# Kernel tuning notes

Hardware: AMD Instinct MI355X
Metric: run time of the kernel (lower is better)

## Reference

```python
import jax, jax.numpy as jnp
import numpy as np

SPATIAL_SCALE = 0.125  # stride-8 FPN level
POINTS = 5


def _sample_points(bb):
    # bb: [N,H,W,5] = (cx, cy, w, h, theta) in image coords
    cx, cy, w, h, t = [bb[..., i] for i in range(5)]
    if POINTS == 1:
        px = cx[..., None]
        py = cy[..., None]
    else:
        vx = w * jnp.cos(t) * 0.5
        vy = w * jnp.sin(t) * 0.5
        wx = -h * jnp.sin(t) * 0.5
        wy = h * jnp.cos(t) * 0.5
        px = jnp.stack([cx, cx + vx + wx, cx - vx + wx, cx - vx - wx, cx + vx - wx], axis=-1)
        py = jnp.stack([cy, cy + vy + wy, cy - vy + wy, cy - vy - wy, cy + vy - wy], axis=-1)
    return px * SPATIAL_SCALE, py * SPATIAL_SCALE  # [N,H,W,P] feature-map coords


def _bilinear_gather(feat, y, x):
    # feat: [N,C,H,W]; y,x: [N,H,W,P] -> [N,H,W,P,C], mmcv-style bilinear w/ border rules
    N, C, H, W = feat.shape
    valid = (y >= -1.0) & (y <= H) & (x >= -1.0) & (x <= W)
    y = jnp.maximum(y, 0.0)
    x = jnp.maximum(x, 0.0)
    y_low = jnp.minimum(jnp.floor(y).astype(jnp.int32), H - 1)
    x_low = jnp.minimum(jnp.floor(x).astype(jnp.int32), W - 1)
    # if low index hits last row/col, snap coordinate onto it (ly/lx = 0)
    y = jnp.where(y_low >= H - 1, y_low.astype(feat.dtype), y)
    x = jnp.where(x_low >= W - 1, x_low.astype(feat.dtype), x)
    y_high = jnp.minimum(y_low + 1, H - 1)
    x_high = jnp.minimum(x_low + 1, W - 1)
    ly = y - y_low.astype(feat.dtype)
    lx = x - x_low.astype(feat.dtype)
    hy = 1.0 - ly
    hx = 1.0 - lx
    nn = jnp.arange(N)[:, None, None, None]  # broadcasts against [N,H,W,P]

    def g(yy, xx):
        return feat[nn, :, yy, xx]  # [N,H,W,P,C]

    val = ((hy * hx)[..., None] * g(y_low, x_low)
           + (hy * lx)[..., None] * g(y_low, x_high)
           + (ly * hx)[..., None] * g(y_high, x_low)
           + (ly * lx)[..., None] * g(y_high, x_high))
    return jnp.where(valid[..., None], val, 0.0)


def feature_refine(features, best_rbboxes):
    px, py = _sample_points(best_rbboxes)
    sampled = _bilinear_gather(features, py, px)       # [N,H,W,P,C]
    acc = sampled.sum(axis=3)                           # [N,H,W,C]
    return features + jnp.transpose(acc, (0, 3, 1, 2))  # [N,C,H,W]


def setup_inputs() -> dict:
    key = jax.random.key(0)
    k1, k2, k3, k4, k5, k6 = jax.random.split(key, 6)
    N, C, H, W = 4, 256, 128, 128
    IMG = 1024.0
    features = jax.random.normal(k1, (N, C, H, W), dtype=jnp.float32)
    cx = jax.random.uniform(k2, (N, H, W), minval=0.0, maxval=IMG)
    cy = jax.random.uniform(k3, (N, H, W), minval=0.0, maxval=IMG)
    bw = jax.random.uniform(k4, (N, H, W), minval=8.0, maxval=128.0)
    bh = jax.random.uniform(k5, (N, H, W), minval=8.0, maxval=128.0)
    th = jax.random.uniform(k6, (N, H, W), minval=-np.pi / 2, maxval=np.pi / 2)
    best_rbboxes = jnp.stack([cx, cy, bw, bh, th], axis=-1)  # [N,H,W,5]
    return {"features": features, "best_rbboxes": best_rbboxes}


def reference(features, best_rbboxes):
    return feature_refine(features, best_rbboxes)
```

## Files before the change

### kernel.cpp

```cpp
#include <hip/hip_runtime.h>


#define N_ 4
#define C_ 256
#define H_ 128
#define W_ 128
#define HW_ (H_ * W_)
#define SCALE 0.125f

typedef unsigned int uint32;

__device__ __forceinline__ uint32 f2bf(float f) {
    uint32 u = __float_as_uint(f);
    u = (u + 0x7FFF + ((u >> 16) & 1)) >> 16;
    return u;
}
__device__ __forceinline__ float blo(uint32 u) { return __uint_as_float(u << 16); }
__device__ __forceinline__ float bhi(uint32 u) { return __uint_as_float(u & 0xFFFF0000u); }

__global__ __launch_bounds__(1024, 8) void nchw2nhwc_geo(const float* __restrict__ in,
                                                         const float* __restrict__ bb,
                                                         uint32* __restrict__ outU,
                                                         uint32* __restrict__ geoG)
{
    __shared__ uint32 tile[64 * 260];
    const int t   = threadIdx.x;
    const int l   = t & 63;
    const int g   = t >> 6;
    const int hw0 = blockIdx.x * 256;
    const int ch  = blockIdx.y;
    const int n   = blockIdx.z;

    if (ch == 0 && t < 256) {
        const int px = n * HW_ + hw0 + t;
        const float* b = bb + (size_t)px * 5;
        const float cx = b[0], cy = b[1], bw = b[2], bh = b[3], th = b[4];
        const float st = sinf(th), ct = cosf(th);
        const float vx = bw * ct * 0.5f, vy = bw * st * 0.5f;
        const float wx = -bh * st * 0.5f, wy = bh * ct * 0.5f;
        const float pxs[5] = {cx, cx + vx + wx, cx - vx + wx, cx - vx - wx, cx + vx - wx};
        const float pys[5] = {cy, cy + vy + wy, cy - vy + wy, cy - vy - wy, cy + vy - wy};
        uint32* gw = geoG + (size_t)px * 32;
#pragma unroll
        for (int p = 0; p < 5; ++p) {
            float x = pxs[p] * SCALE;
            float y = pys[p] * SCALE;
            const bool valid = (y >= -1.0f) && (y <= (float)H_) &&
                               (x >= -1.0f) && (x <= (float)W_);
            y = fmaxf(y, 0.0f);
            x = fmaxf(x, 0.0f);
            int yl = min((int)y, H_ - 1);
            int xl = min((int)x, W_ - 1);
            if (yl >= H_ - 1) y = (float)yl;
            if (xl >= W_ - 1) x = (float)xl;
            const int yh = min(yl + 1, H_ - 1);
            const float ly = y - (float)yl, lx = x - (float)xl;
            const float hy = 1.0f - ly,     hx = 1.0f - lx;
            const int xa = min(xl, W_ - 2);
            float wA, wB;
            if (xl < W_ - 1) { wA = hx; wB = lx; }
            else             { wA = 0.0f; wB = 1.0f; }
            const float v = valid ? 1.0f : 0.0f;
            gw[p]      = (uint32)(yl * W_ + xa);
            gw[5 + p]  = (uint32)(yh * W_ + xa);
            gw[10 + p] = __float_as_uint(v * hy * wA);
            gw[15 + p] = __float_as_uint(v * hy * wB);
            gw[20 + p] = __float_as_uint(v * ly * wA);
            gw[25 + p] = __float_as_uint(v * ly * wB);
        }
        gw[30] = 0u; gw[31] = 0u;
    }

    const float* base = in + (size_t)n * C_ * HW_ + (size_t)(ch * 128) * HW_ + hw0 + 4 * l;
    float4 v0[4], v1[4];
#pragma unroll
    for (int r = 0; r < 4; ++r) {
        const int cp = g * 4 + r;
        v0[r] = *(const float4*)(base + (size_t)(2 * cp) * HW_);
        v1[r] = *(const float4*)(base + (size_t)(2 * cp + 1) * HW_);
    }
#pragma unroll
    for (int r = 0; r < 4; ++r) {
        const int cp = g * 4 + r;
        uint4 u;
        u.x = f2bf(v0[r].x) | (f2bf(v1[r].x) << 16);
        u.y = f2bf(v0[r].y) | (f2bf(v1[r].y) << 16);
        u.z = f2bf(v0[r].z) | (f2bf(v1[r].z) << 16);
        u.w = f2bf(v0[r].w) | (f2bf(v1[r].w) << 16);
        *(uint4*)&tile[cp * 260 + 4 * l] = u;
    }
    __syncthreads();
    uint32* dst = outU + ((size_t)n * HW_ + hw0) * 128 + ch * 64;
#pragma unroll
    for (int it = 0; it < 16; ++it) {
        const int f   = it * 1024 + t;
        const int row = f >> 6;
        const int q   = f & 63;
        dst[(size_t)row * 128 + q] = tile[q * 260 + row];
    }
}

__global__ __launch_bounds__(256, 8) void fr_refine(const uint32* __restrict__ nhwcU,
                                                    const uint32* __restrict__ geoG,
                                                    float* __restrict__ out)
{
    __shared__ float tile[32 * 128];
    const int t  = threadIdx.x;
    const int l  = t & 63;
    const int wv = __builtin_amdgcn_readfirstlane(t >> 6);
    const int bx = blockIdx.x;
    const int xcd = bx & 7;
    const int n   = xcd >> 1;
    const int ch  = xcd & 1;
    const int s   = bx >> 3;
    const int h   = s >> 2;
    const int w0  = (s & 3) * 32;

    const int chB = ch << 8;
    const int laneb = ((l & 15) << 4) + (((l >> 4) & 1) << 9);
    const bool hi = (l >= 32);
    const bool b4 = ((l >> 4) & 1) != 0;
    const int hwb = h * W_ + w0 + wv * 8;
    const uint32* gb = geoG + ((size_t)n * HW_ + hwb) * 32;
    const char* plane = (const char*)(nhwcU + (size_t)n * HW_ * 128);

#pragma unroll 1
    for (int p = 0; p < 8; ++p) {
        const uint32* g = gb + p * 32;

        int o0b[5], o1b[5];
        float w00[5], w01[5], w10[5], w11[5];
#pragma unroll
        for (int q = 0; q < 5; ++q) {
            o0b[q] = (int)__builtin_amdgcn_readfirstlane(g[q])     * 512 + chB;
            o1b[q] = (int)__builtin_amdgcn_readfirstlane(g[5 + q]) * 512 + chB;
            w00[q] = __uint_as_float(__builtin_amdgcn_readfirstlane(g[10 + q]));
            w01[q] = __uint_as_float(__builtin_amdgcn_readfirstlane(g[15 + q]));
            w10[q] = __uint_as_float(__builtin_amdgcn_readfirstlane(g[20 + q]));
            w11[q] = __uint_as_float(__builtin_amdgcn_readfirstlane(g[25 + q]));
        }

        uint4 rid = make_uint4(0u, 0u, 0u, 0u);
        if (l < 16)
            rid = *(const uint4*)(plane + (size_t)(hwb + p) * 512 + chB + ((l & 15) << 4));
        uint4 r[5];
#pragma unroll
        for (int q = 0; q < 5; ++q) {
            const int vof = (hi ? o1b[q] : o0b[q]) + laneb;
            r[q] = *(const uint4*)(plane + vof);
        }
        __builtin_amdgcn_sched_barrier(0);

        float a[8];
        a[0] = blo(rid.x); a[1] = bhi(rid.x);
        a[2] = blo(rid.y); a[3] = bhi(rid.y);
        a[4] = blo(rid.z); a[5] = bhi(rid.z);
        a[6] = blo(rid.w); a[7] = bhi(rid.w);
#pragma unroll
        for (int q = 0; q < 5; ++q) {
            const float wq = hi ? (b4 ? w11[q] : w10[q]) : (b4 ? w01[q] : w00[q]);
            a[0] = fmaf(wq, blo(r[q].x), a[0]); a[1] = fmaf(wq, bhi(r[q].x), a[1]);
            a[2] = fmaf(wq, blo(r[q].y), a[2]); a[3] = fmaf(wq, bhi(r[q].y), a[3]);
            a[4] = fmaf(wq, blo(r[q].z), a[4]); a[5] = fmaf(wq, bhi(r[q].z), a[5]);
            a[6] = fmaf(wq, blo(r[q].w), a[6]); a[7] = fmaf(wq, bhi(r[q].w), a[7]);
        }
#pragma unroll
        for (int k = 0; k < 8; ++k) {
            a[k] += __shfl_xor(a[k], 16, 64);
            a[k] += __shfl_xor(a[k], 32, 64);
        }
        if (l < 16) {
            const int px  = wv * 8 + p;
            const int swz = (px & 7) << 2;
            float* base = &tile[px * 128];
            *(float4*)&base[(l * 8) ^ swz]     = make_float4(a[0], a[1], a[2], a[3]);
            *(float4*)&base[(l * 8 + 4) ^ swz] = make_float4(a[4], a[5], a[6], a[7]);
        }
    }
    __syncthreads();
    const size_t obase = (size_t)n * C_ * HW_ + (size_t)(ch * 128) * HW_ + h * W_ + w0;
#pragma unroll
    for (int it = 0; it < 16; ++it) {
        const int flat = it * 256 + t;
        const int px = flat & 31;
        const int c  = flat >> 5;
        out[obase + (size_t)c * HW_ + px] = tile[px * 128 + (c ^ ((px & 7) << 2))];
    }
}

__global__ __launch_bounds__(256) void fr_kernel(
    const float* __restrict__ feat,
    const float* __restrict__ bb,
    float* __restrict__ out)
{
    const int lane = threadIdx.x & 63;
    const int wave = threadIdx.x >> 6;
    const int tile = blockIdx.x;
    const int wt   = tile & 1;
    const int h    = (tile >> 1) & (H_ - 1);
    const int n    = tile >> 8;
    const int w    = wt * 64 + lane;
    const int cb   = blockIdx.y;

    const float* b = bb + (size_t)((n * H_ + h) * W_ + w) * 5;
    const float cx = b[0], cy = b[1], bw = b[2], bh = b[3], th = b[4];
    const float st = sinf(th), ct = cosf(th);
    const float vx = bw * ct * 0.5f, vy = bw * st * 0.5f;
    const float wx = -bh * st * 0.5f, wy = bh * ct * 0.5f;
    const float pxs[5] = {cx, cx + vx + wx, cx - vx + wx, cx - vx - wx, cx + vx - wx};
    const float pys[5] = {cy, cy + vy + wy, cy - vy + wy, cy - vy - wy, cy + vy - wy};

    int   off0[5], off1[5];
    float wgt[20];
#pragma unroll
    for (int p = 0; p < 5; ++p) {
        float x = pxs[p] * SCALE;
        float y = pys[p] * SCALE;
        const bool valid = (y >= -1.0f) && (y <= (float)H_) &&
                           (x >= -1.0f) && (x <= (float)W_);
        y = fmaxf(y, 0.0f);
        x = fmaxf(x, 0.0f);
        int yl = min((int)y, H_ - 1);
        int xl = min((int)x, W_ - 1);
        if (yl >= H_ - 1) y = (float)yl;
        if (xl >= W_ - 1) x = (float)xl;
        const int yh = min(yl + 1, H_ - 1);
        const float ly = y - (float)yl, lx = x - (float)xl;
        const float hy = 1.0f - ly,     hx = 1.0f - lx;
        const int xa = min(xl, W_ - 2);
        float wA, wB;
        if (xl < W_ - 1) { wA = hx; wB = lx; }
        else             { wA = 0.0f; wB = 1.0f; }
        const float v = valid ? 1.0f : 0.0f;
        off0[p] = yl * W_ + xa;
        off1[p] = yh * W_ + xa;
        wgt[p * 4 + 0] = v * hy * wA;
        wgt[p * 4 + 1] = v * hy * wB;
        wgt[p * 4 + 2] = v * ly * wA;
        wgt[p * 4 + 3] = v * ly * wB;
    }

    const int hw = h * W_ + w;
    const size_t planeBase = ((size_t)n * C_ + cb * 64 + wave * 16) * HW_;
    const float* fp = feat + planeBase;
    float*       op = out  + planeBase;
    for (int it = 0; it < 16; ++it) {
        float acc = fp[hw];
#pragma unroll
        for (int p = 0; p < 5; ++p) {
            acc += wgt[p * 4 + 0] * fp[off0[p]]
                 + wgt[p * 4 + 1] * fp[off0[p] + 1]
                 + wgt[p * 4 + 2] * fp[off1[p]]
                 + wgt[p * 4 + 3] * fp[off1[p] + 1];
        }
        op[hw] = acc;
        fp += HW_;
        op += HW_;
    }
}

extern "C" void kernel_launch(void* const* d_in, const int* in_sizes, int n_in,
                              void* d_out, int out_size, void* d_ws, size_t ws_size,
                              hipStream_t stream) {
    const float* feat = (const float*)d_in[0];
    const float* bbox = (const float*)d_in[1];
    float* out = (float*)d_out;

    const size_t nhwcBytes = (size_t)N_ * HW_ * C_ * 2;
    const size_t geoBytes  = (size_t)N_ * HW_ * 32 * 4;
    if (ws_size >= nhwcBytes + geoBytes) {
        uint32* nhwcU = (uint32*)d_ws;
        uint32* geoG  = (uint32*)((char*)d_ws + nhwcBytes);
        nchw2nhwc_geo<<<dim3(HW_ / 256, 2, N_), dim3(1024), 0, stream>>>(feat, bbox, nhwcU, geoG);
        fr_refine<<<dim3(N_ * H_ * (W_ / 32) * 2), dim3(256), 0, stream>>>(nhwcU, geoG, out);
    } else {
        dim3 grid(N_ * H_ * (W_ / 64), C_ / 64, 1);
        fr_kernel<<<grid, dim3(256), 0, stream>>>(feat, bbox, out);
    }
}
```

Baseline: 158.6 us.

## Store per-corner byte offsets and weights interleaved; use per-lane vector loads and packed FMA

The geometry record is changed from a 32-word struct-of-arrays to 40 words per pixel, laid out as (byte offset, weight) pairs per corner with offsets pre-multiplied by 512. In the refine kernel each lane now loads its own uint2 offset/weight pair directly, replacing 30 scalar readfirstlane loads and the per-lane select chains. Accumulation is written with 2-wide float vectors so the compiler can emit packed FMA instructions. The price is a larger geometry buffer (160 vs 128 bytes per pixel) and vector rather than scalar loads of the geometry.

```diff
diff --git a/kernel.cpp b/kernel.cpp
--- a/kernel.cpp
+++ b/kernel.cpp
@@ -9,6 +9,7 @@
 #define SCALE 0.125f
 
 typedef unsigned int uint32;
+typedef float f32x2 __attribute__((ext_vector_type(2)));
 
 __device__ __forceinline__ uint32 f2bf(float f) {
     uint32 u = __float_as_uint(f);
@@ -40,7 +41,7 @@
         const float wx = -bh * st * 0.5f, wy = bh * ct * 0.5f;
         const float pxs[5] = {cx, cx + vx + wx, cx - vx + wx, cx - vx - wx, cx + vx - wx};
         const float pys[5] = {cy, cy + vy + wy, cy - vy + wy, cy - vy - wy, cy + vy - wy};
-        uint32* gw = geoG + (size_t)px * 32;
+        uint32* gw = geoG + (size_t)px * 40;
 #pragma unroll
         for (int p = 0; p < 5; ++p) {
             float x = pxs[p] * SCALE;
@@ -61,14 +62,17 @@
             if (xl < W_ - 1) { wA = hx; wB = lx; }
             else             { wA = 0.0f; wB = 1.0f; }
             const float v = valid ? 1.0f : 0.0f;
-            gw[p]      = (uint32)(yl * W_ + xa);
-            gw[5 + p]  = (uint32)(yh * W_ + xa);
-            gw[10 + p] = __float_as_uint(v * hy * wA);
-            gw[15 + p] = __float_as_uint(v * hy * wB);
-            gw[20 + p] = __float_as_uint(v * ly * wA);
-            gw[25 + p] = __float_as_uint(v * ly * wB);
-        }
-        gw[30] = 0u; gw[31] = 0u;
+            const int pix0 = yl * W_ + xa;
+            const int pix1 = yh * W_ + xa;
+            *(uint4*)&gw[p * 8]     = make_uint4((uint32)(pix0 * 512),
+                                                 __float_as_uint(v * hy * wA),
+                                                 (uint32)((pix0 + 1) * 512),
+                                                 __float_as_uint(v * hy * wB));
+            *(uint4*)&gw[p * 8 + 4] = make_uint4((uint32)(pix1 * 512),
+                                                 __float_as_uint(v * ly * wA),
+                                                 (uint32)((pix1 + 1) * 512),
+                                                 __float_as_uint(v * ly * wB));
+        }
     }
 
     const float* base = in + (size_t)n * C_ * HW_ + (size_t)(ch * 128) * HW_ + hw0 + 4 * l;
@@ -116,54 +120,47 @@
     const int h   = s >> 2;
     const int w0  = (s & 3) * 32;
 
-    const int chB = ch << 8;
-    const int laneb = ((l & 15) << 4) + (((l >> 4) & 1) << 9);
-    const bool hi = (l >= 32);
-    const bool b4 = ((l >> 4) & 1) != 0;
-    const int hwb = h * W_ + w0 + wv * 8;
-    const uint32* gb = geoG + ((size_t)n * HW_ + hwb) * 32;
-    const char* plane = (const char*)(nhwcU + (size_t)n * HW_ * 128);
+    const int k8   = (l >> 4) << 3;
+    const int slot = (l & 15) << 4;
+    const int hwb  = h * W_ + w0 + wv * 8;
+    const char* gbase = (const char*)geoG + (size_t)(n * HW_ + hwb) * 160;
+    const char* plane = (const char*)(nhwcU + (size_t)n * HW_ * 128) + (ch << 8);
 
 #pragma unroll 1
     for (int p = 0; p < 8; ++p) {
-        const uint32* g = gb + p * 32;
-
-        int o0b[5], o1b[5];
-        float w00[5], w01[5], w10[5], w11[5];
-#pragma unroll
-        for (int q = 0; q < 5; ++q) {
-            o0b[q] = (int)__builtin_amdgcn_readfirstlane(g[q])     * 512 + chB;
-            o1b[q] = (int)__builtin_amdgcn_readfirstlane(g[5 + q]) * 512 + chB;
-            w00[q] = __uint_as_float(__builtin_amdgcn_readfirstlane(g[10 + q]));
-            w01[q] = __uint_as_float(__builtin_amdgcn_readfirstlane(g[15 + q]));
-            w10[q] = __uint_as_float(__builtin_amdgcn_readfirstlane(g[20 + q]));
-            w11[q] = __uint_as_float(__builtin_amdgcn_readfirstlane(g[25 + q]));
-        }
+        const char* gq = gbase + p * 160;
+
+        uint2 ow[5];
+#pragma unroll
+        for (int q = 0; q < 5; ++q)
+            ow[q] = *(const uint2*)(gq + q * 32 + k8);
 
         uint4 rid = make_uint4(0u, 0u, 0u, 0u);
         if (l < 16)
-            rid = *(const uint4*)(plane + (size_t)(hwb + p) * 512 + chB + ((l & 15) << 4));
+            rid = *(const uint4*)(plane + (size_t)(hwb + p) * 512 + slot);
         uint4 r[5];
 #pragma unroll
+        for (int q = 0; q < 5; ++q)
+            r[q] = *(const uint4*)(plane + ow[q].x + slot);
+        __builtin_amdgcn_sched_barrier(0);
+
+        f32x2 acc0, acc1, acc2, acc3;
+        acc0.x = blo(rid.x); acc0.y = bhi(rid.x);
+        acc1.x = blo(rid.y); acc1.y = bhi(rid.y);
+        acc2.x = blo(rid.z); acc2.y = bhi(rid.z);
+        acc3.x = blo(rid.w); acc3.y = bhi(rid.w);
+#pragma unroll
         for (int q = 0; q < 5; ++q) {
-            const int vof = (hi ? o1b[q] : o0b[q]) + laneb;
-            r[q] = *(const uint4*)(plane + vof);
-        }
-        __builtin_amdgcn_sched_barrier(0);
-
-        float a[8];
-        a[0] = blo(rid.x); a[1] = bhi(rid.x);
-        a[2] = blo(rid.y); a[3] = bhi(rid.y);
-        a[4] = blo(rid.z); a[5] = bhi(rid.z);
-        a[6] = blo(rid.w); a[7] = bhi(rid.w);
-#pragma unroll
-        for (int q = 0; q < 5; ++q) {
-            const float wq = hi ? (b4 ? w11[q] : w10[q]) : (b4 ? w01[q] : w00[q]);
-            a[0] = fmaf(wq, blo(r[q].x), a[0]); a[1] = fmaf(wq, bhi(r[q].x), a[1]);
-            a[2] = fmaf(wq, blo(r[q].y), a[2]); a[3] = fmaf(wq, bhi(r[q].y), a[3]);
-            a[4] = fmaf(wq, blo(r[q].z), a[4]); a[5] = fmaf(wq, bhi(r[q].z), a[5]);
-            a[6] = fmaf(wq, blo(r[q].w), a[6]); a[7] = fmaf(wq, bhi(r[q].w), a[7]);
-        }
+            const float w = __uint_as_float(ow[q].y);
+            f32x2 w2; w2.x = w; w2.y = w;
+            f32x2 u;
+            u.x = blo(r[q].x); u.y = bhi(r[q].x); acc0 += u * w2;
+            u.x = blo(r[q].y); u.y = bhi(r[q].y); acc1 += u * w2;
+            u.x = blo(r[q].z); u.y = bhi(r[q].z); acc2 += u * w2;
+            u.x = blo(r[q].w); u.y = bhi(r[q].w); acc3 += u * w2;
+        }
+        float a[8] = {acc0.x, acc0.y, acc1.x, acc1.y,
+                      acc2.x, acc2.y, acc3.x, acc3.y};
 #pragma unroll
         for (int k = 0; k < 8; ++k) {
             a[k] += __shfl_xor(a[k], 16, 64);
@@ -267,7 +264,7 @@
     float* out = (float*)d_out;
 
     const size_t nhwcBytes = (size_t)N_ * HW_ * C_ * 2;
-    const size_t geoBytes  = (size_t)N_ * HW_ * 32 * 4;
+    const size_t geoBytes  = (size_t)N_ * HW_ * 160;
     if (ws_size >= nhwcBytes + geoBytes) {
         uint32* nhwcU = (uint32*)d_ws;
         uint32* geoG  = (uint32*)((char*)d_ws + nhwcBytes);
```

Measured after the change: 167.4 us. +5.5%, slower.
